# Optimization experiments

Measured on AMD Instinct MI355X. Metric: run time of the kernel, lower is better.

The kernel has to match this reference:

```python
import jax, jax.numpy as jnp
import numpy as np

B, S, D, H = 2, 2048, 1024, 16
HD = D // H  # 64
EPS = 1e-6


def setup_inputs() -> dict:
    key = jax.random.key(0)
    ks = jax.random.split(key, 12)
    s = 1.0 / np.sqrt(D)
    return {
        "query": jax.random.normal(ks[0], (B, S, D), jnp.float32),
        "key": jax.random.normal(ks[1], (B, S, D), jnp.float32),
        "value": jax.random.normal(ks[2], (B, S, D), jnp.float32),
        "mask": jax.random.randint(ks[3], (B, S, S), 0, 2) == 1,
        "Wq": jax.random.normal(ks[4], (D, D), jnp.float32) * s,
        "bq": jnp.zeros((D,), jnp.float32),
        "Wk": jax.random.normal(ks[5], (D, D), jnp.float32) * s,
        "bk": jnp.zeros((D,), jnp.float32),
        "Wv": jax.random.normal(ks[6], (D, D), jnp.float32) * s,
        "bv": jnp.zeros((D,), jnp.float32),
        "Wo": jax.random.normal(ks[7], (D, D), jnp.float32) * s,
        "bo": jnp.zeros((D,), jnp.float32),
        "gamma": jnp.ones((D,), jnp.float32),
        "beta": jnp.zeros((D,), jnp.float32),
    }


def reference(query, key, value, mask, Wq, bq, Wk, bk, Wv, bv, Wo, bo, gamma, beta):
    b, sq, _ = query.shape
    sk = key.shape[1]
    # QKV projections -> [b, h, s, hd]
    q = (query @ Wq + bq).reshape(b, sq, H, HD).transpose(0, 2, 1, 3)
    k = (key @ Wk + bk).reshape(b, sk, H, HD).transpose(0, 2, 1, 3)
    v = (value @ Wv + bv).reshape(b, sk, H, HD).transpose(0, 2, 1, 3)
    # scores [b, h, sq, sk]
    scores = jnp.einsum("bhqd,bhkd->bhqk", q, k) / jnp.sqrt(jnp.float32(HD))
    scores = jnp.where(mask[:, None, :, :], -jnp.inf, scores)
    attn = jax.nn.softmax(scores, axis=-1)  # dropout: eval mode (identity)
    out = jnp.einsum("bhqk,bhkd->bhqd", attn, v)
    out = out.transpose(0, 2, 1, 3).reshape(b, sq, H * HD)
    out = out @ Wo + bo
    # residual + LayerNorm with unbiased std and (std + eps) denominator (faithful to torch code)
    x = query + out
    mean = x.mean(-1, keepdims=True)
    std = jnp.std(x, axis=-1, keepdims=True, ddof=1)
    return gamma * (x - mean) / (std + EPS) + beta
```

## Files before the change

kernel.cpp:

```cpp
#include <hip/hip_runtime.h>


#define NB 2
#define SS 2048
#define DDIM 1024
#define NH 16
#define HDIM 64
#define MROWS (NB * SS)

typedef unsigned short u16;
typedef unsigned long long u64;
typedef unsigned int u32;
typedef short bf16x8 __attribute__((ext_vector_type(8)));
typedef float f32x4 __attribute__((ext_vector_type(4)));

typedef const __attribute__((address_space(1))) void GASV;
typedef __attribute__((address_space(3))) void LASV;

__device__ __forceinline__ float dev_exp2(float x) {
  float r;
  asm("v_exp_f32 %0, %1" : "=v"(r) : "v"(x));
  return r;
}

__device__ __forceinline__ u16 f2bf(float f) {
  unsigned u = __builtin_bit_cast(unsigned, f);
  u += 0x7FFFu + ((u >> 16) & 1u);
  return (u16)(u >> 16);
}

__device__ __forceinline__ u32 cvt_pk_bf16(float a, float b) {
  u32 d;
  asm("v_cvt_pk_bf16_f32 %0, %1, %2" : "=v"(d) : "v"(a), "v"(b));
  return d;
}

__global__ __launch_bounds__(256) void cvt_bf16_3(const float* __restrict__ q,
                                                  const float* __restrict__ k,
                                                  const float* __restrict__ v,
                                                  u16* __restrict__ out) {
  const float* in = (blockIdx.y == 0) ? q : (blockIdx.y == 1) ? k : v;
  size_t i = ((size_t)blockIdx.x * 256 + threadIdx.x) * 4;
  float4 val = *(const float4*)(in + i);
  uint2 o;
  u16* po = (u16*)&o;
  po[0] = f2bf(val.x); po[1] = f2bf(val.y); po[2] = f2bf(val.z); po[3] = f2bf(val.w);
  *(uint2*)(out + (size_t)blockIdx.y * MROWS * DDIM + i) = o;
}

__global__ __launch_bounds__(256) void cvt_mask_bits(const int* __restrict__ in,
                                                     u64* __restrict__ out) {
  size_t w = ((size_t)blockIdx.x * 256 + threadIdx.x) >> 6;
  int lane = threadIdx.x & 63;
  int v = in[w * 64 + lane];
  u64 bits = __ballot(v != 0);
  if (lane == 0) out[w] = bits;
}

__global__ __launch_bounds__(256) void transpose_cvt_w4(const float* __restrict__ W0,
                                                        const float* __restrict__ W1,
                                                        const float* __restrict__ W2,
                                                        const float* __restrict__ W3,
                                                        u16* __restrict__ WTbase) {
  __shared__ u16 t[64][65];
  const int z = blockIdx.z;
  const float* W = (z == 0) ? W0 : (z == 1) ? W1 : (z == 2) ? W2 : W3;
  u16* WT = WTbase + (size_t)z * DDIM * DDIM;
  const int k0 = blockIdx.x * 64, n0 = blockIdx.y * 64;
  const int tid = threadIdx.x;
  const int r = tid >> 4;
  const int c4 = (tid & 15) * 4;
#pragma unroll
  for (int it = 0; it < 4; ++it) {
    int k = r + it * 16;
    float4 v = *(const float4*)&W[(size_t)(k0 + k) * DDIM + n0 + c4];
    t[c4 + 0][k] = f2bf(v.x);
    t[c4 + 1][k] = f2bf(v.y);
    t[c4 + 2][k] = f2bf(v.z);
    t[c4 + 3][k] = f2bf(v.w);
  }
  __syncthreads();
#pragma unroll
  for (int it = 0; it < 4; ++it) {
    int n = r + it * 16;
    uint2 o;
    u16* po = (u16*)&o;
#pragma unroll
    for (int j = 0; j < 4; ++j) po[j] = t[n][c4 + j];
    *(uint2*)&WT[(size_t)(n0 + n) * DDIM + k0 + c4] = o;
  }
}

template <int MODE>
__global__ __launch_bounds__(256) void gemm_bt(const u16* __restrict__ Abase,
                                               const u16* __restrict__ BT,
                                               const float* __restrict__ b0,
                                               const float* __restrict__ b1,
                                               const float* __restrict__ b2,
                                               const float* __restrict__ resid,
                                               void* __restrict__ C,
                                               void* __restrict__ Cv) {
  __shared__ __align__(16) u16 SMEM[2][2][128][64];
  u16(&Al)[2][128][64] = SMEM[0];
  u16(&Bl)[2][128][64] = SMEM[1];
  const int tid = threadIdx.x;
  const int wid = tid >> 6, lane = tid & 63;
  const int wm = (wid >> 1) * 64, wn = (wid & 1) * 64;
  const int NCOL = (MODE == 0) ? 24 : 8;
  const int lin = blockIdx.y * 32 + blockIdx.x;
  const int xcd = lin & 7, idx = lin >> 3;
  const int rowA0 = (xcd * 4 + idx / NCOL) * 128;
  const int colB0 = (idx % NCOL) * 128;
  const int sel = (MODE == 0) ? (colB0 >> 10) : 0;
  const u16* Ag = Abase + (size_t)sel * ((size_t)MROWS * DDIM) + (size_t)rowA0 * DDIM;
  const u16* Bg = BT + (size_t)colB0 * DDIM;
  f32x4 acc[4][4] = {};
  const int rl = lane >> 3;
  const int ce = (lane & 7) * 8;

#define G_STAGE(buf, kt)                                                       \
  do {                                                                         \
    _Pragma("unroll") for (int c = 0; c < 4; ++c) {                            \
      int rt = wid * 32 + c * 8;                                               \
      __builtin_amdgcn_global_load_lds(                                        \
          (GASV*)(Ag + (size_t)(rt + rl) * DDIM + (kt) + ce),                  \
          (LASV*)((char*)&Al[buf][0][0] + rt * 128), 16, 0, 0);                \
      __builtin_amdgcn_global_load_lds(                                        \
          (GASV*)(Bg + (size_t)(rt + rl) * DDIM + (kt) + ce),                  \
          (LASV*)((char*)&Bl[buf][0][0] + rt * 128), 16, 0, 0);                \
    }                                                                          \
  } while (0)

  G_STAGE(0, 0);
  __syncthreads();
  for (int t = 0; t < 16; ++t) {
    const int cur = t & 1;
    if (t < 15) G_STAGE(cur ^ 1, (t + 1) * 64);
#pragma unroll
    for (int kk = 0; kk < 64; kk += 32) {
      bf16x8 af[4], bfr[4];
#pragma unroll
      for (int i = 0; i < 4; ++i)
        af[i] = *(const bf16x8*)&Al[cur][wm + i * 16 + (lane & 15)][kk + (lane >> 4) * 8];
#pragma unroll
      for (int j = 0; j < 4; ++j)
        bfr[j] = *(const bf16x8*)&Bl[cur][wn + j * 16 + (lane & 15)][kk + (lane >> 4) * 8];
#pragma unroll
      for (int i = 0; i < 4; ++i)
#pragma unroll
        for (int j = 0; j < 4; ++j)
          acc[i][j] = __builtin_amdgcn_mfma_f32_16x16x32_bf16(af[i], bfr[j], acc[i][j], 0, 0, 0);
    }
    __syncthreads();
  }
#undef G_STAGE

  const int cb = lane & 15, hi = lane >> 4;
  if (MODE == 0) {
    if (sel == 2) {
      u16(*T)[136] = (u16(*)[136]) & SMEM[0][0][0][0];
      const int dcol0 = colB0 & 1023;
#pragma unroll
      for (int j = 0; j < 4; ++j) {
        int dl = wn + j * 16 + cb;
        float bv = b2[dcol0 + dl];
#pragma unroll
        for (int i = 0; i < 4; ++i) {
          int sl = wm + i * 16 + hi * 4;
          uint2 o;
          o.x = cvt_pk_bf16(acc[i][j][0] + bv, acc[i][j][1] + bv);
          o.y = cvt_pk_bf16(acc[i][j][2] + bv, acc[i][j][3] + bv);
          *(uint2*)&T[dl][sl] = o;
        }
      }
      __syncthreads();
      const int bb = rowA0 >> 11, s0 = rowA0 & (SS - 1);
#pragma unroll
      for (int it = 0; it < 8; ++it) {
        int chunk = it * 256 + tid;
        int dl = chunk >> 4;
        int sc = (chunk & 15) * 8;
        int dg = dcol0 + dl;
        *(bf16x8*)&((u16*)Cv)[((size_t)(bb * NH + (dg >> 6)) * HDIM + (dg & 63)) * SS +
                              s0 + sc] = *(const bf16x8*)&T[dl][sc];
      }
    } else {
      const float* bp = (sel == 0) ? b0 : b1;
      const float scale = (sel == 0) ? 0.125f * 1.44269504088896340736f : 1.0f;
      u16* dst = (u16*)C + (size_t)sel * ((size_t)MROWS * DDIM);
      const int colw0 = (colB0 & 1023) + wn;
#pragma unroll
      for (int i = 0; i < 4; ++i)
#pragma unroll
        for (int j = 0; j < 4; ++j) {
          int colw = colw0 + j * 16 + cb;
          float bv = bp[colw];
#pragma unroll
          for (int r = 0; r < 4; ++r) {
            int row = rowA0 + wm + i * 16 + hi * 4 + r;
            dst[(size_t)row * DDIM + colw] = f2bf((acc[i][j][r] + bv) * scale);
          }
        }
    }
  } else {
#pragma unroll
    for (int i = 0; i < 4; ++i)
#pragma unroll
      for (int j = 0; j < 4; ++j) {
        int col = colB0 + wn + j * 16 + cb;
        float bv = b0[col];
#pragma unroll
        for (int r = 0; r < 4; ++r) {
          int row = rowA0 + wm + i * 16 + hi * 4 + r;
          size_t off = (size_t)row * DDIM + col;
          ((float*)C)[off] = acc[i][j][r] + bv + resid[off];
        }
      }
  }
}

__global__ __launch_bounds__(512, 6) void attn_fwd(const u16* __restrict__ Qp,
                                                   const u16* __restrict__ Kp,
                                                   const u16* __restrict__ VpT,
                                                   const u64* __restrict__ Mbits,
                                                   u16* __restrict__ O) {
  __shared__ __align__(16) u16 Kl[2][64][64];
  __shared__ __align__(16) u16 Vl[2][64][64];
  __shared__ __align__(16) u16 Pl[8][16][64];
  const int tid = threadIdx.x, wid = tid >> 6, lane = tid & 63;
  const int bid = blockIdx.x;
  const int bh = (bid & 7) * 4 + ((bid >> 3) & 3);
  const int q0 = (bid >> 5) * 128;
  const int b = bh >> 4, h = bh & 15;
  const int hi = lane >> 4, cbase = lane & 15, lx = lane & 7;

  bf16x8 qf[2];
  {
    const u16* qb = Qp + (size_t)(b * SS + q0 + wid * 16 + cbase) * DDIM + h * 64 + hi * 8;
    qf[0] = *(const bf16x8*)qb;
    qf[1] = *(const bf16x8*)(qb + 32);
  }
  const bf16x8 ONES8 = {(short)0x3F80, (short)0x3F80, (short)0x3F80, (short)0x3F80,
                        (short)0x3F80, (short)0x3F80, (short)0x3F80, (short)0x3F80};
  f32x4 l_acc = (f32x4){0.f, 0.f, 0.f, 0.f};
  f32x4 accO[4];
#pragma unroll
  for (int f = 0; f < 4; ++f) accO[f] = (f32x4){0.f, 0.f, 0.f, 0.f};

  const u16* Kgb = Kp + (size_t)b * SS * DDIM + h * 64;
  const u16* Vgb = VpT + (size_t)bh * 64 * SS;
  const u64* Mb = Mbits + (size_t)(b * SS + q0 + wid * 16 + cbase) * (SS / 64);
  const int rl = lane >> 3;
  const int ceS = ((lane & 7) ^ rl) * 8;

  int fo[4][2];
#pragma unroll
  for (int f = 0; f < 4; ++f)
#pragma unroll
    for (int ks = 0; ks < 2; ++ks)
      fo[f][ks] = (f * 16 + cbase) * 64 + (((ks * 4 + hi) ^ lx) << 3);
  int pw[4];
#pragma unroll
  for (int f = 0; f < 4; ++f)
    pw[f] = cbase * 64 + (((f * 2 + (hi >> 1)) ^ lx) << 3) + ((hi & 1) << 2);
  u16* KlF = &Kl[0][0][0];
  u16* VlF = &Vl[0][0][0];
  u16* Plw = &Pl[wid][0][0];

#define STAGE_KV(BUF, kv)                                                      \
  do {                                                                         \
    int rt = wid * 8;                                                          \
    __builtin_amdgcn_global_load_lds(                                          \
        (GASV*)(Kgb + (size_t)((kv) + rt + rl) * DDIM + ceS),                  \
        (LASV*)((char*)KlF + (BUF) * 8192 + rt * 128), 16, 0, 0);              \
    __builtin_amdgcn_global_load_lds(                                          \
        (GASV*)(Vgb + (size_t)(rt + rl) * SS + (kv) + ceS),                    \
        (LASV*)((char*)VlF + (BUF) * 8192 + rt * 128), 16, 0, 0);              \
  } while (0)

#define ATTN_ITER(T, CUR, DO_STAGE, MROW)                                      \
  do {                                                                         \
    if (DO_STAGE) STAGE_KV((CUR) ^ 1, ((T) + 1) * 64);                         \
    f32x4 sc[4];                                                               \
    __builtin_amdgcn_s_setprio(1);                                             \
    _Pragma("unroll") for (int fn = 0; fn < 4; ++fn) {                         \
      f32x4 c = (f32x4){0.f, 0.f, 0.f, 0.f};                                   \
      _Pragma("unroll") for (int ks = 0; ks < 2; ++ks) {                       \
        bf16x8 kf = *(const bf16x8*)(KlF + (CUR) * 4096 + fo[fn][ks]);         \
        c = __builtin_amdgcn_mfma_f32_16x16x32_bf16(kf, qf[ks], c, 0, 0, 0);   \
      }                                                                        \
      sc[fn] = c;                                                              \
    }                                                                          \
    __builtin_amdgcn_s_setprio(0);                                             \
             \
    u64 mh = (MROW) >> (hi * 4);                                               \
    u32 mlo = (u32)mh, mhi2 = (u32)(mh >> 32);                                 \
    _Pragma("unroll") for (int fn = 0; fn < 4; ++fn) {                         \
      u32 b4 = ((fn < 2) ? mlo : mhi2) >> ((fn & 1) * 16);                     \
      _Pragma("unroll") for (int j = 0; j < 4; ++j) {                          \
        float bf_ = (float)((b4 >> j) & 1u);                                   \
        sc[fn][j] = dev_exp2(fmaf(bf_, -512.f, sc[fn][j]));                    \
      }                                                                        \
    }                                                                          \
    _Pragma("unroll") for (int fn = 0; fn < 4; ++fn) {                         \
      uint2 wpair;                                                             \
      wpair.x = cvt_pk_bf16(sc[fn][0], sc[fn][1]);                             \
      wpair.y = cvt_pk_bf16(sc[fn][2], sc[fn][3]);                             \
      *(uint2*)(Plw + pw[fn]) = wpair;                                         \
    }                                                                          \
    bf16x8 pf0 = *(const bf16x8*)(Plw + fo[0][0]);                             \
    bf16x8 pf1 = *(const bf16x8*)(Plw + fo[0][1]);                             \
    __builtin_amdgcn_s_setprio(1);                                             \
    l_acc = __builtin_amdgcn_mfma_f32_16x16x32_bf16(pf0, ONES8, l_acc, 0, 0, 0); \
    l_acc = __builtin_amdgcn_mfma_f32_16x16x32_bf16(pf1, ONES8, l_acc, 0, 0, 0); \
    _Pragma("unroll") for (int nd = 0; nd < 4; ++nd) {                         \
      bf16x8 v0 = *(const bf16x8*)(VlF + (CUR) * 4096 + fo[nd][0]);            \
      bf16x8 v1 = *(const bf16x8*)(VlF + (CUR) * 4096 + fo[nd][1]);            \
      accO[nd] = __builtin_amdgcn_mfma_f32_16x16x32_bf16(pf0, v0, accO[nd], 0, 0, 0); \
      accO[nd] = __builtin_amdgcn_mfma_f32_16x16x32_bf16(pf1, v1, accO[nd], 0, 0, 0); \
    }                                                                          \
    __builtin_amdgcn_s_setprio(0);                                             \
    __syncthreads();                                                           \
  } while (0)

  STAGE_KV(0, 0);
  __syncthreads();
  for (int th = 0; th < 16; ++th) {
    uint4 mw = *(const uint4*)&Mb[2 * th];
    u64 m0 = ((u64)mw.y << 32) | mw.x;
    u64 m1 = ((u64)mw.w << 32) | mw.z;
    ATTN_ITER(2 * th, 0, true, m0);
    ATTN_ITER(2 * th + 1, 1, (th != 15), m1);
  }
#undef ATTN_ITER
#undef STAGE_KV

#pragma unroll
  for (int nd = 0; nd < 4; ++nd)
#pragma unroll
    for (int j = 0; j < 4; ++j) {
      int row = q0 + wid * 16 + hi * 4 + j;
      int col = h * 64 + nd * 16 + cbase;
      O[(size_t)(b * SS + row) * DDIM + col] = f2bf(accO[nd][j] / l_acc[j]);
    }
}

__global__ __launch_bounds__(256) void ln_res(const float* __restrict__ xin,
                                              const float* __restrict__ gamma,
                                              const float* __restrict__ beta,
                                              float* __restrict__ out) {
  const int tid = threadIdx.x, wid = tid >> 6, lane = tid & 63;
  const int row = blockIdx.x * 4 + wid;
  const float* xr = xin + (size_t)row * DDIM;
  float4 x[4];
  float s = 0.f;
#pragma unroll
  for (int i = 0; i < 4; ++i) {
    x[i] = *(const float4*)(xr + lane * 4 + i * 256);
    s += (x[i].x + x[i].y) + (x[i].z + x[i].w);
  }
#pragma unroll
  for (int off = 32; off >= 1; off >>= 1) s += __shfl_xor(s, off, 64);
  float mean = s * (1.0f / DDIM);
  float ss = 0.f;
#pragma unroll
  for (int i = 0; i < 4; ++i) {
    x[i].x -= mean; x[i].y -= mean; x[i].z -= mean; x[i].w -= mean;
    ss += (x[i].x * x[i].x + x[i].y * x[i].y) + (x[i].z * x[i].z + x[i].w * x[i].w);
  }
#pragma unroll
  for (int off = 32; off >= 1; off >>= 1) ss += __shfl_xor(ss, off, 64);
  float var = ss * (1.0f / (DDIM - 1));
  float rden = 1.0f / (sqrtf(var) + 1e-6f);
  float* orow = out + (size_t)row * DDIM;
#pragma unroll
  for (int i = 0; i < 4; ++i) {
    float4 g = *(const float4*)(gamma + lane * 4 + i * 256);
    float4 be = *(const float4*)(beta + lane * 4 + i * 256);
    float4 o;
    o.x = g.x * x[i].x * rden + be.x;
    o.y = g.y * x[i].y * rden + be.y;
    o.z = g.z * x[i].z * rden + be.z;
    o.w = g.w * x[i].w * rden + be.w;
    *(float4*)(orow + lane * 4 + i * 256) = o;
  }
}

extern "C" void kernel_launch(void* const* d_in, const int* in_sizes, int n_in,
                              void* d_out, int out_size, void* d_ws, size_t ws_size,
                              hipStream_t stream) {
  const float* query = (const float*)d_in[0];
  const float* key = (const float*)d_in[1];
  const float* value = (const float*)d_in[2];
  const int* mask = (const int*)d_in[3];
  const float* Wq = (const float*)d_in[4];
  const float* bq = (const float*)d_in[5];
  const float* Wk = (const float*)d_in[6];
  const float* bk = (const float*)d_in[7];
  const float* Wv = (const float*)d_in[8];
  const float* bv = (const float*)d_in[9];
  const float* Wo = (const float*)d_in[10];
  const float* bo = (const float*)d_in[11];
  const float* gamma = (const float*)d_in[12];
  const float* beta = (const float*)d_in[13];
  float* out = (float*)d_out;
  char* ws = (char*)d_ws;
  const size_t MB = 1ull << 20;
  u16* qkvb = (u16*)(ws + 0 * MB);
  u16* WT = (u16*)(ws + 24 * MB);
  u16* WoT = (u16*)(ws + 30 * MB);
  u16* Qp = (u16*)(ws + 32 * MB);
  u16* Kp = (u16*)(ws + 40 * MB);
  u16* VpT = (u16*)(ws + 48 * MB);
  u16* attnb = (u16*)(ws + 56 * MB);
  u64* maskbits = (u64*)(ws + 0 * MB);
  float* proj = (float*)(ws + 8 * MB);

  cvt_bf16_3<<<dim3(MROWS * DDIM / 1024, 3), 256, 0, stream>>>(query, key, value, qkvb);
  transpose_cvt_w4<<<dim3(16, 16, 4), 256, 0, stream>>>(Wq, Wk, Wv, Wo, WT);
  gemm_bt<0><<<dim3(32, 24), 256, 0, stream>>>(qkvb, WT, bq, bk, bv, nullptr, Qp, VpT);
  cvt_mask_bits<<<(NB * SS * SS) / 256, 256, 0, stream>>>(mask, maskbits);
  attn_fwd<<<512, 512, 0, stream>>>(Qp, Kp, VpT, maskbits, attnb);
  gemm_bt<1><<<dim3(32, 8), 256, 0, stream>>>(attnb, WoT, bo, nullptr, nullptr,
                                              query, proj, nullptr);
  ln_res<<<MROWS / 4, 256, 0, stream>>>(proj, gamma, beta, out);
}
```

Baseline: 155.8 us.

## Triple-buffer K/V tiles in attention with vmcnt waits and one barrier

Result: no change. 153.2 us (-1.7%).

```diff
diff --git a/kernel.cpp b/kernel.cpp
--- a/kernel.cpp
+++ b/kernel.cpp
@@ -219,13 +219,13 @@
   }
 }
 
-__global__ __launch_bounds__(512, 6) void attn_fwd(const u16* __restrict__ Qp,
+__global__ __launch_bounds__(512, 4) void attn_fwd(const u16* __restrict__ Qp,
                                                    const u16* __restrict__ Kp,
                                                    const u16* __restrict__ VpT,
                                                    const u64* __restrict__ Mbits,
                                                    u16* __restrict__ O) {
-  __shared__ __align__(16) u16 Kl[2][64][64];
-  __shared__ __align__(16) u16 Vl[2][64][64];
+  __shared__ __align__(16) u16 Kl[3][64][64];
+  __shared__ __align__(16) u16 Vl[3][64][64];
   __shared__ __align__(16) u16 Pl[8][16][64];
   const int tid = threadIdx.x, wid = tid >> 6, lane = tid & 63;
   const int bid = blockIdx.x;
@@ -278,22 +278,27 @@
         (LASV*)((char*)VlF + (BUF) * 8192 + rt * 128), 16, 0, 0);              \
   } while (0)
 
-#define ATTN_ITER(T, CUR, DO_STAGE, MROW)                                      \
+#define WAITVM(N) asm volatile("s_waitcnt vmcnt(" #N ")" ::: "memory")
+
+#define ATTN_ITER(T, BUF, DO_STAGE, VM)                                        \
   do {                                                                         \
-    if (DO_STAGE) STAGE_KV((CUR) ^ 1, ((T) + 1) * 64);                         \
+    WAITVM(VM);                                                                \
+    __builtin_amdgcn_s_barrier();                                              \
+    u64 mrow = Mb[T];                                                          \
+    if (DO_STAGE) STAGE_KV(((BUF) + 2) % 3, ((T) + 2) * 64);                   \
     f32x4 sc[4];                                                               \
     __builtin_amdgcn_s_setprio(1);                                             \
     _Pragma("unroll") for (int fn = 0; fn < 4; ++fn) {                         \
       f32x4 c = (f32x4){0.f, 0.f, 0.f, 0.f};                                   \
       _Pragma("unroll") for (int ks = 0; ks < 2; ++ks) {                       \
-        bf16x8 kf = *(const bf16x8*)(KlF + (CUR) * 4096 + fo[fn][ks]);         \
+        bf16x8 kf = *(const bf16x8*)(KlF + (BUF) * 4096 + fo[fn][ks]);         \
         c = __builtin_amdgcn_mfma_f32_16x16x32_bf16(kf, qf[ks], c, 0, 0, 0);   \
       }                                                                        \
       sc[fn] = c;                                                              \
     }                                                                          \
     __builtin_amdgcn_s_setprio(0);                                             \
              \
-    u64 mh = (MROW) >> (hi * 4);                                               \
+    u64 mh = mrow >> (hi * 4);                                                 \
     u32 mlo = (u32)mh, mhi2 = (u32)(mh >> 32);                                 \
     _Pragma("unroll") for (int fn = 0; fn < 4; ++fn) {                         \
       u32 b4 = ((fn < 2) ? mlo : mhi2) >> ((fn & 1) * 16);                     \
@@ -314,25 +319,25 @@
     l_acc = __builtin_amdgcn_mfma_f32_16x16x32_bf16(pf0, ONES8, l_acc, 0, 0, 0); \
     l_acc = __builtin_amdgcn_mfma_f32_16x16x32_bf16(pf1, ONES8, l_acc, 0, 0, 0); \
     _Pragma("unroll") for (int nd = 0; nd < 4; ++nd) {                         \
-      bf16x8 v0 = *(const bf16x8*)(VlF + (CUR) * 4096 + fo[nd][0]);            \
-      bf16x8 v1 = *(const bf16x8*)(VlF + (CUR) * 4096 + fo[nd][1]);            \
+      bf16x8 v0 = *(const bf16x8*)(VlF + (BUF) * 4096 + fo[nd][0]);            \
+      bf16x8 v1 = *(const bf16x8*)(VlF + (BUF) * 4096 + fo[nd][1]);            \
       accO[nd] = __builtin_amdgcn_mfma_f32_16x16x32_bf16(pf0, v0, accO[nd], 0, 0, 0); \
       accO[nd] = __builtin_amdgcn_mfma_f32_16x16x32_bf16(pf1, v1, accO[nd], 0, 0, 0); \
     }                                                                          \
     __builtin_amdgcn_s_setprio(0);                                             \
-    __syncthreads();                                                           \
   } while (0)
 
   STAGE_KV(0, 0);
-  __syncthreads();
-  for (int th = 0; th < 16; ++th) {
-    uint4 mw = *(const uint4*)&Mb[2 * th];
-    u64 m0 = ((u64)mw.y << 32) | mw.x;
-    u64 m1 = ((u64)mw.w << 32) | mw.z;
-    ATTN_ITER(2 * th, 0, true, m0);
-    ATTN_ITER(2 * th + 1, 1, (th != 15), m1);
-  }
+  STAGE_KV(1, 64);
+  for (int t3 = 0; t3 < 30; t3 += 3) {
+    ATTN_ITER(t3 + 0, 0, true, 2);
+    ATTN_ITER(t3 + 1, 1, true, 2);
+    ATTN_ITER(t3 + 2, 2, true, 2);
+  }
+  ATTN_ITER(30, 0, false, 2);
+  ATTN_ITER(31, 1, false, 0);
 #undef ATTN_ITER
+#undef WAITVM
 #undef STAGE_KV
 
 #pragma unroll
```
